# Kernel tuning notes

Hardware: AMD Instinct MI355X
Metric: run time of the kernel (lower is better)

Reference implementation:

```python
import jax, jax.numpy as jnp
import numpy as np

B, T, DIM, NH = 4, 2048, 1024, 16
HD = DIM // NH


def setup_inputs() -> dict:
    key = jax.random.key(0)
    ks = jax.random.split(key, 9)
    s = 0.02
    return {
        "x": jax.random.normal(ks[0], (B, T, DIM), dtype=jnp.float32),
        "Wq": jax.random.normal(ks[1], (DIM, DIM), dtype=jnp.float32) * s,
        "bq": jnp.zeros((DIM,), dtype=jnp.float32),
        "Wk": jax.random.normal(ks[2], (DIM, DIM), dtype=jnp.float32) * s,
        "bk": jnp.zeros((DIM,), dtype=jnp.float32),
        "Wv": jax.random.normal(ks[3], (DIM, DIM), dtype=jnp.float32) * s,
        "bv": jnp.zeros((DIM,), dtype=jnp.float32),
        "Wo": jax.random.normal(ks[4], (DIM, DIM), dtype=jnp.float32) * s,
        "bo": jnp.zeros((DIM,), dtype=jnp.float32),
    }


def reference(x, Wq, bq, Wk, bk, Wv, bv, Wo, bo):
    scale = HD ** -0.5
    # QKV projections (torch Linear: x @ W.T + b; here W stored as [in, out])
    q = (x @ Wq + bq).reshape(B, T, NH, HD).transpose(0, 2, 1, 3)  # [B,H,T,D]
    k = (x @ Wk + bk).reshape(B, T, NH, HD).transpose(0, 2, 1, 3)
    v = (x @ Wv + bv).reshape(B, T, NH, HD).transpose(0, 2, 1, 3)
    scores = jnp.einsum("bhqd,bhkd->bhqk", q, k) * scale  # [B,H,T,T]
    attn = jax.nn.softmax(scores, axis=-1)
    out = jnp.einsum("bhqk,bhkd->bhqd", attn, v)  # [B,H,T,D]
    out = out.transpose(0, 2, 1, 3).reshape(B, T, DIM)
    return out @ Wo + bo
```

## Files before the change

kernel.cpp:

```cpp
#include <hip/hip_runtime.h>
#include <math.h>

#define BB   4
#define TT   2048
#define DIMM 1024
#define NHH  16
#define HDD  64
#define MM   (BB * TT)

typedef unsigned short u16;
typedef unsigned int   u32;
typedef short bf16x8 __attribute__((ext_vector_type(8)));
typedef float f32x4  __attribute__((ext_vector_type(4)));

__device__ __forceinline__ u16 f2bf(float f) {
    u32 u = __float_as_uint(f);
    return (u16)((u + 0x7fffu + ((u >> 16) & 1u)) >> 16);
}

__device__ __forceinline__ f32x4 mfma16(bf16x8 a, bf16x8 b, f32x4 c) {
    return __builtin_amdgcn_mfma_f32_16x16x32_bf16(a, b, c, 0, 0, 0);
}

__device__ __forceinline__ int swz8(int row, int slot) {
    return ((slot ^ (row & 7) ^ ((row >> 3) & 7)) & 7) * 8;
}
__device__ __forceinline__ int swz4(int row, int slot) {
    return ((slot ^ (row & 3)) & 3) * 8;
}

__global__ void convert_x_bf16(const float* __restrict__ in, u16* __restrict__ out) {
    int i = (blockIdx.x * 256 + threadIdx.x) * 8;
    float4 a = *(const float4*)(in + i);
    float4 b = *(const float4*)(in + i + 4);
    u32 w0 = f2bf(a.x) | ((u32)f2bf(a.y) << 16);
    u32 w1 = f2bf(a.z) | ((u32)f2bf(a.w) << 16);
    u32 w2 = f2bf(b.x) | ((u32)f2bf(b.y) << 16);
    u32 w3 = f2bf(b.z) | ((u32)f2bf(b.w) << 16);
    uint4 o = make_uint4(w0, w1, w2, w3);
    *(uint4*)(out + i) = o;
}

__global__ void transpose_w_bf16(const float* __restrict__ W, u16* __restrict__ Wt) {
    __shared__ float tile[32][33];
    const int c  = threadIdx.x & 31;
    const int r8 = threadIdx.x >> 5;
    const int kb = blockIdx.y * 32, nb = blockIdx.x * 32;
#pragma unroll
    for (int rr = 0; rr < 4; ++rr) {
        int r = r8 + rr * 8;
        tile[r][c] = W[(kb + r) * 1024 + nb + c];
    }
    __syncthreads();
#pragma unroll
    for (int rr = 0; rr < 4; ++rr) {
        int r = r8 + rr * 8;
        Wt[(nb + r) * 1024 + kb + c] = f2bf(tile[c][r]);
    }
}

template <int OLAYOUT>
__global__ __launch_bounds__(256, 2) void gemm_bf16(
    const u16* __restrict__ A, const u16* __restrict__ Bt,
    const float* __restrict__ bias, void* __restrict__ Cout, float oscale)
{
    __shared__ u16 As[128 * 32];
    __shared__ u16 Bs[128 * 32];

    const int tid  = threadIdx.x;
    const int m0   = blockIdx.x * 128;
    const int n0   = blockIdx.y * 128;
    const int wave = tid >> 6, lane = tid & 63;
    const int wr = wave >> 1, wc = wave & 1;
    const int l15 = lane & 15, l4 = lane >> 4;

    const int r0 = tid >> 2, ks = tid & 3;
    const int r1 = r0 + 64;
    const int w0 = r0 * 32 + swz4(r0, ks);
    const int w1 = r1 * 32 + swz4(r1, ks);

    f32x4 acc[4][4];
#pragma unroll
    for (int i = 0; i < 4; ++i)
#pragma unroll
        for (int j = 0; j < 4; ++j) acc[i][j] = (f32x4){0.f, 0.f, 0.f, 0.f};

    const u16* Ar0 = A  + (m0 + r0) * 1024 + ks * 8;
    const u16* Ar1 = A  + (m0 + r1) * 1024 + ks * 8;
    const u16* Br0 = Bt + (n0 + r0) * 1024 + ks * 8;
    const u16* Br1 = Bt + (n0 + r1) * 1024 + ks * 8;

    uint4 a0 = *(const uint4*)Ar0;
    uint4 a1 = *(const uint4*)Ar1;
    uint4 b0 = *(const uint4*)Br0;
    uint4 b1 = *(const uint4*)Br1;
    *(uint4*)&As[w0] = a0; *(uint4*)&As[w1] = a1;
    *(uint4*)&Bs[w0] = b0; *(uint4*)&Bs[w1] = b1;
    __syncthreads();

    for (int kt = 0; kt < 32; ++kt) {
        if (kt < 31) {
            const int ko = (kt + 1) * 32;
            a0 = *(const uint4*)(Ar0 + ko);
            a1 = *(const uint4*)(Ar1 + ko);
            b0 = *(const uint4*)(Br0 + ko);
            b1 = *(const uint4*)(Br1 + ko);
        }
        bf16x8 af[4], bf[4];
#pragma unroll
        for (int rt = 0; rt < 4; ++rt) {
            int row = wr * 64 + rt * 16 + l15;
            af[rt] = *(const bf16x8*)&As[row * 32 + swz4(row, l4)];
            int col = wc * 64 + rt * 16 + l15;
            bf[rt] = *(const bf16x8*)&Bs[col * 32 + swz4(col, l4)];
        }
#pragma unroll
        for (int rt = 0; rt < 4; ++rt)
#pragma unroll
            for (int ct = 0; ct < 4; ++ct)
                acc[rt][ct] = mfma16(af[rt], bf[ct], acc[rt][ct]);
        __syncthreads();
        if (kt < 31) {
            *(uint4*)&As[w0] = a0; *(uint4*)&As[w1] = a1;
            *(uint4*)&Bs[w0] = b0; *(uint4*)&Bs[w1] = b1;
            __syncthreads();
        }
    }

#pragma unroll
    for (int rt = 0; rt < 4; ++rt)
#pragma unroll
        for (int ct = 0; ct < 4; ++ct) {
            int n = n0 + wc * 64 + ct * 16 + l15;
            float bn = bias[n];
            if (OLAYOUT == 2) {
                int m00 = m0 + wr * 64 + rt * 16 + l4 * 4;
                int b = m00 >> 11, t0 = m00 & 2047;
                int h = n >> 6, d = n & 63;
                ushort4 pk;
                pk.x = f2bf((acc[rt][ct][0] + bn) * oscale);
                pk.y = f2bf((acc[rt][ct][1] + bn) * oscale);
                pk.z = f2bf((acc[rt][ct][2] + bn) * oscale);
                pk.w = f2bf((acc[rt][ct][3] + bn) * oscale);
                *(ushort4*)(&((u16*)Cout)[((((b << 4) + h) * 64 + d) << 11) + t0]) = pk;
            } else {
#pragma unroll
                for (int i = 0; i < 4; ++i) {
                    int m = m0 + wr * 64 + rt * 16 + l4 * 4 + i;
                    float v = (acc[rt][ct][i] + bn) * oscale;
                    if (OLAYOUT == 0) {
                        ((float*)Cout)[m * 1024 + n] = v;
                    } else {
                        int b = m >> 11, t = m & 2047;
                        int h = n >> 6,  d = n & 63;
                        ((u16*)Cout)[(((b << 4) + h) * 2048 + t) * 64 + d] = f2bf(v);
                    }
                }
            }
        }
}

__global__ __launch_bounds__(256, 4) void attn_mfma(
    const u16* __restrict__ Qb, const u16* __restrict__ Kb,
    const u16* __restrict__ Vtg, u16* __restrict__ Ob)
{
    __shared__ u16 Ks[2][64 * 64];
    __shared__ u16 Vts[2][64 * 64];
    __shared__ u16 Ps[4][16 * 64];

    const int tid   = threadIdx.x;
    const int g     = blockIdx.x;
    const int chunk = (g & 7) * 256 + (g >> 3);
    const int bh    = chunk >> 5;
    const int q0    = (chunk & 31) * 64;
    const int b     = bh >> 4, h = bh & 15;
    const u16* Qp   = Qb + (bh * TT + q0) * HDD;
    const u16* Kp   = Kb + bh * TT * HDD;
    const u16* Vp   = Vtg + bh * TT * HDD;

    const int wave = tid >> 6, lane = tid & 63;
    const int l15 = lane & 15, l4 = lane >> 4;

    bf16x8 qf[2];
#pragma unroll
    for (int hf = 0; hf < 2; ++hf)
        qf[hf] = *(const bf16x8*)(Qp + (wave * 16 + l15) * HDD + hf * 32 + l4 * 8);

    f32x4 oacc[4];
    float mr = -INFINITY, lr = 0.f;
#pragma unroll
    for (int db = 0; db < 4; ++db) oacc[db] = (f32x4){0.f, 0.f, 0.f, 0.f};

    const int r0 = tid >> 3, ds = tid & 7;
    const int r1 = r0 + 32;
    const int wo0 = r0 * 64 + swz8(r0, ds);
    const int wo1 = r1 * 64 + swz8(r1, ds);

    uint4 kr0, kr1, vr0, vr1;
    kr0 = *(const uint4*)(Kp + r0 * 64 + ds * 8);
    kr1 = *(const uint4*)(Kp + r1 * 64 + ds * 8);
    vr0 = *(const uint4*)(Vp + r0 * 2048 + ds * 8);
    vr1 = *(const uint4*)(Vp + r1 * 2048 + ds * 8);
    *(uint4*)&Ks[0][wo0]  = kr0;
    *(uint4*)&Ks[0][wo1]  = kr1;
    *(uint4*)&Vts[0][wo0] = vr0;
    *(uint4*)&Vts[0][wo1] = vr1;
    __syncthreads();

    for (int kv = 0; kv < TT / 64; ++kv) {
        const int cur = kv & 1;

        if (kv < TT / 64 - 1) {
            const u16* Kt = Kp + (kv + 1) * 64 * HDD;
            const u16* Vt = Vp + (kv + 1) * 64;
            kr0 = *(const uint4*)(Kt + r0 * 64 + ds * 8);
            kr1 = *(const uint4*)(Kt + r1 * 64 + ds * 8);
            vr0 = *(const uint4*)(Vt + r0 * 2048 + ds * 8);
            vr1 = *(const uint4*)(Vt + r1 * 2048 + ds * 8);
        }

        f32x4 sacc[4];
#pragma unroll
        for (int nt = 0; nt < 4; ++nt) sacc[nt] = (f32x4){0.f, 0.f, 0.f, 0.f};
        __builtin_amdgcn_s_setprio(1);
#pragma unroll
        for (int nt = 0; nt < 4; ++nt) {
            int krow = nt * 16 + l15;
#pragma unroll
            for (int hf = 0; hf < 2; ++hf) {
                bf16x8 kf = *(const bf16x8*)&Ks[cur][krow * 64 + swz8(krow, hf * 4 + l4)];
                sacc[nt] = mfma16(kf, qf[hf], sacc[nt]);
            }
        }
        __builtin_amdgcn_s_setprio(0);

        float mx = sacc[0][0];
#pragma unroll
        for (int nt = 0; nt < 4; ++nt)
#pragma unroll
            for (int i = 0; i < 4; ++i) mx = fmaxf(mx, sacc[nt][i]);
        mx = fmaxf(mx, __shfl_xor(mx, 16, 64));
        mx = fmaxf(mx, __shfl_xor(mx, 32, 64));

        if (__any(mx > mr + 8.f)) {
            float mnew = fmaxf(mr, mx);
            float rsc  = exp2f(mr - mnew);
            mr = mnew;
            lr *= rsc;
            float rr[4];
#pragma unroll
            for (int i = 0; i < 4; ++i) rr[i] = __shfl(rsc, l4 * 4 + i, 16);
#pragma unroll
            for (int db = 0; db < 4; ++db)
#pragma unroll
                for (int i = 0; i < 4; ++i) oacc[db][i] *= rr[i];
        }

        float lsum = 0.f;
        {
            u32* Pw = (u32*)&Ps[wave][0];
#pragma unroll
            for (int nt = 0; nt < 4; ++nt)
#pragma unroll
                for (int p = 0; p < 2; ++p) {
                    float pa = exp2f(sacc[nt][2 * p]     - mr);
                    float pb = exp2f(sacc[nt][2 * p + 1] - mr);
                    lsum += pa + pb;
                    u32 pk = (u32)f2bf(pa) | ((u32)f2bf(pb) << 16);
                    int k2   = nt * 16 + l4 * 4 + 2 * p;
                    int slot = k2 >> 3;
                    int phys = l15 * 64 + (((slot ^ (l15 & 7)) & 7) << 3) + (k2 & 7);
                    Pw[phys >> 1] = pk;
                }
        }
        lsum += __shfl_xor(lsum, 16, 64);
        lsum += __shfl_xor(lsum, 32, 64);
        lr += lsum;

        bf16x8 pf[2];
#pragma unroll
        for (int hf = 0; hf < 2; ++hf) {
            int slot = hf * 4 + l4;
            pf[hf] = *(const bf16x8*)&Ps[wave][l15 * 64 + (((slot ^ (l15 & 7)) & 7) << 3)];
        }
        __builtin_amdgcn_s_setprio(1);
#pragma unroll
        for (int db = 0; db < 4; ++db) {
            int d = db * 16 + l15;
#pragma unroll
            for (int hf = 0; hf < 2; ++hf) {
                bf16x8 vf = *(const bf16x8*)&Vts[cur][d * 64 + swz8(d, hf * 4 + l4)];
                oacc[db] = mfma16(pf[hf], vf, oacc[db]);
            }
        }
        __builtin_amdgcn_s_setprio(0);

        if (kv < TT / 64 - 1) {
            const int nxt = cur ^ 1;
            *(uint4*)&Ks[nxt][wo0]  = kr0;
            *(uint4*)&Ks[nxt][wo1]  = kr1;
            *(uint4*)&Vts[nxt][wo0] = vr0;
            *(uint4*)&Vts[nxt][wo1] = vr1;
        }
        __syncthreads();
    }

    float inv[4];
#pragma unroll
    for (int i = 0; i < 4; ++i) inv[i] = 1.f / __shfl(lr, l4 * 4 + i, 16);
#pragma unroll
    for (int db = 0; db < 4; ++db)
#pragma unroll
        for (int i = 0; i < 4; ++i) {
            int t   = q0 + wave * 16 + l4 * 4 + i;
            int col = h * 64 + db * 16 + l15;
            Ob[(b * TT + t) * DIMM + col] = f2bf(oacc[db][i] * inv[i]);
        }
}

extern "C" void kernel_launch(void* const* d_in, const int* in_sizes, int n_in,
                              void* d_out, int out_size, void* d_ws, size_t ws_size,
                              hipStream_t stream)
{
    const float* x  = (const float*)d_in[0];
    const float* Wq = (const float*)d_in[1];
    const float* bq = (const float*)d_in[2];
    const float* Wk = (const float*)d_in[3];
    const float* bk = (const float*)d_in[4];
    const float* Wv = (const float*)d_in[5];
    const float* bv = (const float*)d_in[6];
    const float* Wo = (const float*)d_in[7];
    const float* bo = (const float*)d_in[8];

    u16* xb   = (u16*)d_ws;
    u16* wqt  = xb   + 8388608;
    u16* wkt  = wqt  + 1048576;
    u16* wvt  = wkt  + 1048576;
    u16* wot  = wvt  + 1048576;
    u16* qbuf = wot  + 1048576;
    u16* obuf = qbuf + 8388608;
    u16* kbuf = (u16*)d_out;
    u16* vbuf = kbuf + 8388608;

    convert_x_bf16<<<4096, 256, 0, stream>>>(x, xb);
    transpose_w_bf16<<<dim3(32, 32), 256, 0, stream>>>(Wq, wqt);
    transpose_w_bf16<<<dim3(32, 32), 256, 0, stream>>>(Wk, wkt);
    transpose_w_bf16<<<dim3(32, 32), 256, 0, stream>>>(Wv, wvt);
    transpose_w_bf16<<<dim3(32, 32), 256, 0, stream>>>(Wo, wot);

    dim3 gg(MM / 128, DIMM / 128);
    const float qscale = 0.125f * 1.44269504f;
    gemm_bf16<1><<<gg, 256, 0, stream>>>(xb, wqt, bq, qbuf, qscale);
    gemm_bf16<1><<<gg, 256, 0, stream>>>(xb, wkt, bk, kbuf, 1.0f);
    gemm_bf16<2><<<gg, 256, 0, stream>>>(xb, wvt, bv, vbuf, 1.0f);

    attn_mfma<<<BB * NHH * (TT / 64), 256, 0, stream>>>(qbuf, kbuf, vbuf, obuf);

    gemm_bf16<0><<<gg, 256, 0, stream>>>(obuf, wot, bo, d_out, 1.0f);
}
```

Measured before the change: 275.1 us.

## Drop per-tile row-max reduction with optimistic exp and overflow-triggered rescale

The attention inner loop no longer computes a row max and cross-lane shuffles on every KV tile. It exponentiates against the running max straight away and only recomputes the max, rescales the accumulator and repacks P when the row sum overflows or turns non-finite. The change also converts P to bf16 with a hardware pack instruction instead of manual rounding, precomputes the LDS write and read offsets for P outside the loop, and changes the P swizzle to avoid bank conflicts. The risk is that P entries can grow very large before a rescale triggers, which relies on fp32/bf16 range and could cost some precision.

```diff
diff --git a/kernel.cpp b/kernel.cpp
--- a/kernel.cpp
+++ b/kernel.cpp
@@ -191,6 +191,22 @@
 #pragma unroll
     for (int db = 0; db < 4; ++db) oacc[db] = (f32x4){0.f, 0.f, 0.f, 0.f};
 
+    const int pxor = (l15 & 7) ^ ((l15 >> 3) << 2);
+    u32* const Pw = (u32*)&Ps[wave][0];
+    int pidx[8];
+#pragma unroll
+    for (int nt = 0; nt < 4; ++nt)
+#pragma unroll
+        for (int pp = 0; pp < 2; ++pp) {
+            int k2 = nt * 16 + l4 * 4 + 2 * pp;
+            int slotW = ((k2 >> 3) ^ pxor) & 7;
+            pidx[nt * 2 + pp] = (l15 * 64 + slotW * 8 + (k2 & 7)) >> 1;
+        }
+    int pread[2];
+#pragma unroll
+    for (int hf = 0; hf < 2; ++hf)
+        pread[hf] = l15 * 64 + ((((hf << 2) + l4) ^ pxor) & 7) * 8;
+
     const int r0 = tid >> 3, ds = tid & 7;
     const int r1 = r0 + 32;
     const int wo0 = r0 * 64 + swz8(r0, ds);
@@ -234,15 +250,32 @@
         }
         __builtin_amdgcn_s_setprio(0);
 
-        float mx = sacc[0][0];
-#pragma unroll
-        for (int nt = 0; nt < 4; ++nt)
-#pragma unroll
-            for (int i = 0; i < 4; ++i) mx = fmaxf(mx, sacc[nt][i]);
-        mx = fmaxf(mx, __shfl_xor(mx, 16, 64));
-        mx = fmaxf(mx, __shfl_xor(mx, 32, 64));
-
-        if (__any(mx > mr + 8.f)) {
+        auto pack_pass = [&]() -> float {
+            float ls = 0.f;
+#pragma unroll
+            for (int nt = 0; nt < 4; ++nt)
+#pragma unroll
+                for (int pp = 0; pp < 2; ++pp) {
+                    float pa = exp2f(sacc[nt][2 * pp]     - mr);
+                    float pb = exp2f(sacc[nt][2 * pp + 1] - mr);
+                    ls += pa + pb;
+                    u32 pk;
+                    asm("v_cvt_pk_bf16_f32 %0, %1, %2" : "=v"(pk) : "v"(pa), "v"(pb));
+                    Pw[pidx[nt * 2 + pp]] = pk;
+                }
+            return ls;
+        };
+        float lsum = pack_pass();
+        float ls2 = lsum + __shfl_xor(lsum, 16, 64);
+        ls2 += __shfl_xor(ls2, 32, 64);
+        if (__builtin_expect(__any(!(ls2 < 1e30f)), 0)) {
+            float mx = sacc[0][0];
+#pragma unroll
+            for (int nt = 0; nt < 4; ++nt)
+#pragma unroll
+                for (int i = 0; i < 4; ++i) mx = fmaxf(mx, sacc[nt][i]);
+            mx = fmaxf(mx, __shfl_xor(mx, 16, 64));
+            mx = fmaxf(mx, __shfl_xor(mx, 32, 64));
             float mnew = fmaxf(mr, mx);
             float rsc  = exp2f(mr - mnew);
             mr = mnew;
@@ -254,35 +287,16 @@
             for (int db = 0; db < 4; ++db)
 #pragma unroll
                 for (int i = 0; i < 4; ++i) oacc[db][i] *= rr[i];
-        }
-
-        float lsum = 0.f;
-        {
-            u32* Pw = (u32*)&Ps[wave][0];
-#pragma unroll
-            for (int nt = 0; nt < 4; ++nt)
-#pragma unroll
-                for (int p = 0; p < 2; ++p) {
-                    float pa = exp2f(sacc[nt][2 * p]     - mr);
-                    float pb = exp2f(sacc[nt][2 * p + 1] - mr);
-                    lsum += pa + pb;
-                    u32 pk = (u32)f2bf(pa) | ((u32)f2bf(pb) << 16);
-                    int k2   = nt * 16 + l4 * 4 + 2 * p;
-                    int slot = k2 >> 3;
-                    int phys = l15 * 64 + (((slot ^ (l15 & 7)) & 7) << 3) + (k2 & 7);
-                    Pw[phys >> 1] = pk;
-                }
-        }
-        lsum += __shfl_xor(lsum, 16, 64);
-        lsum += __shfl_xor(lsum, 32, 64);
-        lr += lsum;
+            lsum = pack_pass();
+            ls2 = lsum + __shfl_xor(lsum, 16, 64);
+            ls2 += __shfl_xor(ls2, 32, 64);
+        }
+        lr += ls2;
 
         bf16x8 pf[2];
 #pragma unroll
-        for (int hf = 0; hf < 2; ++hf) {
-            int slot = hf * 4 + l4;
-            pf[hf] = *(const bf16x8*)&Ps[wave][l15 * 64 + (((slot ^ (l15 & 7)) & 7) << 3)];
-        }
+        for (int hf = 0; hf < 2; ++hf)
+            pf[hf] = *(const bf16x8*)&Ps[wave][pread[hf]];
         __builtin_amdgcn_s_setprio(1);
 #pragma unroll
         for (int db = 0; db < 4; ++db) {
```

After: 257.7 us. -6.3%, faster.
